# Optimization experiments

Hardware: AMD Instinct MI355X
Metric: run time of the kernel (lower is better)

The kernel has to match this reference:

```python
import jax, jax.numpy as jnp
import numpy as np

T = 512        # sentence length
V = 50000      # word vocab
NT = 50        # tag vocab
WD = 200       # word_dims
TD = 50        # tag_dims
U = 512        # lstm_units (per direction)
HID = 1024     # hidden_units
SOUT = 2       # struct_out
LOUT = 56      # label_out
NS = 8192      # number of struct span-sets
NL = 8192      # number of label span-sets
KS = 4         # struct_spans
KL = 3         # label_spans


def _spans(kl, kr, n, k):
    lefts = jax.random.randint(kl, (n, k), 1, T - 2)
    rights = jnp.minimum(lefts + jax.random.randint(kr, (n, k), 0, 16), T - 2)
    return lefts.astype(jnp.int32), rights.astype(jnp.int32)


def setup_inputs() -> dict:
    key = jax.random.key(0)
    ks = jax.random.split(key, 40)
    s = 0.02
    inp = {
        'word_inds': jax.random.randint(ks[0], (T,), 0, V).astype(jnp.int32),
        'tag_inds': jax.random.randint(ks[1], (T,), 0, NT).astype(jnp.int32),
        'struct_targets': jax.random.randint(ks[2], (NS,), 0, SOUT).astype(jnp.int32),
        'label_targets': jax.random.randint(ks[3], (NL,), 0, LOUT).astype(jnp.int32),
    }
    inp['struct_lefts'], inp['struct_rights'] = _spans(ks[4], ks[5], NS, KS)
    inp['label_lefts'], inp['label_rights'] = _spans(ks[6], ks[7], NL, KL)
    inp['W_word'] = jax.random.normal(ks[8], (V, WD), jnp.float32) * s
    inp['W_tag'] = jax.random.normal(ks[9], (NT, TD), jnp.float32) * s
    # LSTM params, PyTorch layout: W_ih [4U, in], W_hh [4U, U], bias [4U] (b_ih+b_hh fused)
    d0, d1 = WD + TD, 2 * U
    i = 10
    for name, din in [('l0f', d0), ('l0b', d0), ('l1f', d1), ('l1b', d1)]:
        inp['Wih_' + name] = jax.random.normal(ks[i], (4 * U, din), jnp.float32) * s; i += 1
        inp['Whh_' + name] = jax.random.normal(ks[i], (4 * U, U), jnp.float32) * s; i += 1
        inp['b_' + name] = jnp.zeros((4 * U,), jnp.float32)
    inp['Ws1'] = jax.random.normal(ks[i], (HID, 2 * KS * U), jnp.float32) * s; i += 1
    inp['bs1'] = jnp.zeros((HID,), jnp.float32)
    inp['Ws2'] = jax.random.normal(ks[i], (SOUT, HID), jnp.float32) * s; i += 1
    inp['bs2'] = jnp.zeros((SOUT,), jnp.float32)
    inp['Wl1'] = jax.random.normal(ks[i], (HID, 2 * KL * U), jnp.float32) * s; i += 1
    inp['bl1'] = jnp.zeros((HID,), jnp.float32)
    inp['Wl2'] = jax.random.normal(ks[i], (LOUT, HID), jnp.float32) * s; i += 1
    inp['bl2'] = jnp.zeros((LOUT,), jnp.float32)
    return inp


def _lstm_dir(x, Wih, Whh, b, reverse):
    # x: [T, Din] -> h sequence [T, U]; gate order i,f,g,o (PyTorch)
    xg = x @ Wih.T + b  # [T, 4U]
    u = Whh.shape[1]
    def step(carry, xt):
        h, c = carry
        g = xt + h @ Whh.T
        gi, gf, gg, go = jnp.split(g, 4)
        i = jax.nn.sigmoid(gi); f = jax.nn.sigmoid(gf)
        gg = jnp.tanh(gg); o = jax.nn.sigmoid(go)
        c = f * c + i * gg
        h = o * jnp.tanh(c)
        return (h, c), h
    init = (jnp.zeros((u,), x.dtype), jnp.zeros((u,), x.dtype))
    _, hs = jax.lax.scan(step, init, xg, reverse=reverse)
    return hs


def _span_loss(fwd, back, lefts, rights, targets, W1, b1, W2, b2):
    n = lefts.shape[0]
    f = fwd[rights] - fwd[lefts - 1]          # [N, K, U]
    bk = back[lefts] - back[rights + 1]       # [N, K, U]
    h = jnp.concatenate([f.reshape(n, -1), bk.reshape(n, -1)], axis=1)
    h = jax.nn.relu(h @ W1.T + b1)
    scores = h @ W2.T + b2
    logp = jax.nn.log_softmax(scores, axis=-1)
    return -jnp.take_along_axis(logp, targets[:, None], axis=1)[:, 0]


def reference(word_inds, tag_inds, struct_lefts, struct_rights, struct_targets,
              label_lefts, label_rights, label_targets,
              W_word, W_tag,
              Wih_l0f, Whh_l0f, b_l0f, Wih_l0b, Whh_l0b, b_l0b,
              Wih_l1f, Whh_l1f, b_l1f, Wih_l1b, Whh_l1b, b_l1b,
              Ws1, bs1, Ws2, bs2, Wl1, bl1, Wl2, bl2):
    x = jnp.concatenate([W_word[word_inds], W_tag[tag_inds]], axis=1)  # [T, WD+TD]
    h0 = jnp.concatenate([_lstm_dir(x, Wih_l0f, Whh_l0f, b_l0f, False),
                          _lstm_dir(x, Wih_l0b, Whh_l0b, b_l0b, True)], axis=1)
    out = jnp.concatenate([_lstm_dir(h0, Wih_l1f, Whh_l1f, b_l1f, False),
                           _lstm_dir(h0, Wih_l1b, Whh_l1b, b_l1b, True)], axis=1)  # [T, 2U]
    fwd, back = out[:, :U], out[:, U:]
    sl = _span_loss(fwd, back, struct_lefts, struct_rights, struct_targets, Ws1, bs1, Ws2, bs2)
    ll = _span_loss(fwd, back, label_lefts, label_rights, label_targets, Wl1, bl1, Wl2, bl2)
    return jnp.concatenate([sl, ll]).mean()
```

## Files before the change

### kernel.cpp

```cpp
#include <hip/hip_runtime.h>

using u16 = unsigned short;
using u32 = unsigned int;
typedef __attribute__((ext_vector_type(8))) short bf16x8;
typedef __attribute__((ext_vector_type(4))) float f32x4;

__device__ __forceinline__ u16 f2b(float f) {
  u32 u = __float_as_uint(f);
  return (u16)((u + 0x7fffu + ((u >> 16) & 1u)) >> 16);
}
__device__ __forceinline__ float b2fs(short v) { return __uint_as_float(((u32)(u16)v) << 16); }

static constexpr size_t HEX_SZ    = (size_t)513 * 512 * 4;
static constexpr size_t OFF_HEXF0 = 0;
static constexpr size_t OFF_HEXB0 = OFF_HEXF0 + HEX_SZ;
static constexpr size_t OFF_HEXF1 = OFF_HEXB0 + HEX_SZ;
static constexpr size_t OFF_HEXB1 = OFF_HEXF1 + HEX_SZ;
static constexpr size_t OFF_LACC  = OFF_HEXB1 + HEX_SZ;
static constexpr size_t ZERO_BYTES= OFF_LACC + 1024;
static constexpr size_t OFF_XB    = ZERO_BYTES;
static constexpr size_t OFF_WIH0F = OFF_XB    + (size_t)512*256*2;
static constexpr size_t OFF_WIH0B = OFF_WIH0F + (size_t)2048*256*2;
static constexpr size_t OFF_WIH1F = OFF_WIH0B + (size_t)2048*256*2;
static constexpr size_t OFF_WIH1B = OFF_WIH1F + (size_t)2048*1024*2;
static constexpr size_t OFF_BSALL = OFF_WIH1B + (size_t)2048*1024*2;
static constexpr size_t OFF_BLALL = OFF_BSALL + (size_t)8192*512*2;
static constexpr size_t OFF_HCAT0 = OFF_BLALL + (size_t)6144*512*2;
static constexpr size_t OFF_HCAT1 = OFF_HCAT0 + (size_t)512*1024*2;
static constexpr size_t OFF_XG0F  = OFF_HCAT1 + (size_t)512*1024*2;
static constexpr size_t OFF_XG0B  = OFF_XG0F  + (size_t)512*2048*4;
static constexpr size_t OFF_XG1F  = OFF_XG0B  + (size_t)512*2048*4;
static constexpr size_t OFF_XG1B  = OFF_XG1F  + (size_t)512*2048*4;
static constexpr size_t OFF_PFS   = OFF_XG1B  + (size_t)512*2048*4;
static constexpr size_t OFF_PBS   = OFF_PFS   + (size_t)512*4096*4;
static constexpr size_t OFF_PFL   = OFF_PBS   + (size_t)512*4096*4;
static constexpr size_t OFF_PBL   = OFF_PFL   + (size_t)512*3072*4;

__global__ __launch_bounds__(64) void k_embed(const int* __restrict__ wi, const int* __restrict__ ti,
                                              const float* __restrict__ Ww, const float* __restrict__ Wt,
                                              u16* __restrict__ x) {
  int t = blockIdx.x;
  int w = wi[t], tg = ti[t];
  for (int c = threadIdx.x; c < 256; c += 64) {
    float v = 0.f;
    if (c < 200) v = Ww[(size_t)w * 200 + c];
    else if (c < 250) v = Wt[(size_t)tg * 50 + (c - 200)];
    x[(size_t)t * 256 + c] = f2b(v);
  }
}

__global__ __launch_bounds__(256) void k_castpad(const float* __restrict__ src, u16* __restrict__ dst,
                                                 int K, int Kp, int total) {
  int i = blockIdx.x * 256 + threadIdx.x;
  if (i >= total) return;
  int n = i / Kp, k = i - n * Kp;
  dst[i] = (k < K) ? f2b(src[(size_t)n * K + k]) : (u16)0;
}

__global__ __launch_bounds__(256) void k_reorder(const float* __restrict__ src, u16* __restrict__ dst,
                                                 int NC, int total) {
  int i = blockIdx.x * 256 + threadIdx.x;
  if (i >= total) return;
  int u = i & 511;
  int nidx = i >> 9;
  int k = nidx >> 10, h = nidx & 1023;
  dst[i] = f2b(src[(size_t)h * NC + k * 512 + u]);
}

#define AST 40
__global__ __launch_bounds__(256) void k_gemm(const u16* __restrict__ A, int lda,
                                              const u16* __restrict__ B, int ldb,
                                              float* __restrict__ C, int ldc,
                                              const float* __restrict__ bias, int K) {
  __shared__ u16 As[128 * AST];
  __shared__ u16 Bs[128 * AST];
  int tid = threadIdx.x;
  int lane = tid & 63, wave = tid >> 6;
  int wm = wave >> 1, wn = wave & 1;
  int m0 = blockIdx.y * 128, n0 = blockIdx.x * 128;
  f32x4 z = {0.f, 0.f, 0.f, 0.f};
  f32x4 acc[4][4];
#pragma unroll
  for (int i = 0; i < 4; ++i)
#pragma unroll
    for (int j = 0; j < 4; ++j) acc[i][j] = z;

  for (int k0 = 0; k0 < K; k0 += 32) {
#pragma unroll
    for (int it = 0; it < 2; ++it) {
      int c = tid + it * 256;
      int row = c >> 2, cc = (c & 3) << 3;
      *(bf16x8*)&As[row * AST + cc] = *(const bf16x8*)&A[(size_t)(m0 + row) * lda + k0 + cc];
      *(bf16x8*)&Bs[row * AST + cc] = *(const bf16x8*)&B[(size_t)(n0 + row) * ldb + k0 + cc];
    }
    __syncthreads();
    int rA = lane & 15, kk = (lane >> 4) << 3;
    bf16x8 af[4], bg[4];
#pragma unroll
    for (int i = 0; i < 4; ++i) {
      af[i] = *(const bf16x8*)&As[(wm * 64 + i * 16 + rA) * AST + kk];
      bg[i] = *(const bf16x8*)&Bs[(wn * 64 + i * 16 + rA) * AST + kk];
    }
#pragma unroll
    for (int i = 0; i < 4; ++i)
#pragma unroll
      for (int j = 0; j < 4; ++j)
        acc[i][j] = __builtin_amdgcn_mfma_f32_16x16x32_bf16(af[i], bg[j], acc[i][j], 0, 0, 0);
    __syncthreads();
  }
  int rg = (lane >> 4) << 2;
#pragma unroll
  for (int i = 0; i < 4; ++i)
#pragma unroll
    for (int j = 0; j < 4; ++j) {
      int n = n0 + wn * 64 + j * 16 + (lane & 15);
      float bv = bias ? bias[n] : 0.f;
#pragma unroll
      for (int r = 0; r < 4; ++r) {
        int m = m0 + wm * 64 + i * 16 + rg + r;
        C[(size_t)m * ldc + n] = acc[i][j][r] + bv;
      }
    }
}

__global__ __launch_bounds__(256, 1) void k_lstm(const float* __restrict__ xg_f, const float* __restrict__ xg_b,
                                                 const float* __restrict__ whh_f, const float* __restrict__ whh_b,
                                                 u32* __restrict__ hex_f, u32* __restrict__ hex_b,
                                                 u16* __restrict__ hcat) {
  __shared__ __align__(16) u16 hshb[512];
  __shared__ float gl[128];
  int bid = blockIdx.x;
  int dir = bid >> 4, slice = bid & 15;
  const float* xg  = dir ? xg_b : xg_f;
  const float* whh = dir ? whh_b : whh_f;
  u32* hex = dir ? hex_b : hex_f;
  int u0 = slice * 32;
  int tid = threadIdx.x;
  int wave = tid >> 6, lane = tid & 63;
  int col = lane & 15, kgrp = lane >> 4;

  bf16x8 bfr[2][16];
#pragma unroll
  for (int ntl = 0; ntl < 2; ++ntl) {
    int n = (2 * wave + ntl) * 16 + col;
    int row = (n >> 5) * 512 + u0 + (n & 31);
    const float* wr = whh + (size_t)row * 512;
#pragma unroll
    for (int kt = 0; kt < 16; ++kt) {
      int k0 = kt * 32 + kgrp * 8;
      f32x4 w0 = *(const f32x4*)&wr[k0];
      f32x4 w1 = *(const f32x4*)&wr[k0 + 4];
      bf16x8 v;
      v[0] = (short)f2b(w0.x); v[1] = (short)f2b(w0.y);
      v[2] = (short)f2b(w0.z); v[3] = (short)f2b(w0.w);
      v[4] = (short)f2b(w1.x); v[5] = (short)f2b(w1.y);
      v[6] = (short)f2b(w1.z); v[7] = (short)f2b(w1.w);
      bfr[ntl][kt] = v;
    }
  }

  float creg = 0.f;
  for (int s = 0; s < 512; ++s) {
    int t = dir ? (511 - s) : s;
    int rrow = dir ? (t + 1) : t;

    float xga = 0.f, xgb2 = 0.f, xgc = 0.f, xgd = 0.f;
    if (tid < 32) {
      const float* xr = &xg[(size_t)t * 2048 + u0 + tid];
      xga = xr[0]; xgb2 = xr[512]; xgc = xr[1024]; xgd = xr[1536];
    }

    for (int i = tid; i < 512; i += 256) {
      u32 w;
      do {
        w = __hip_atomic_load(&hex[(size_t)rrow * 512 + i], __ATOMIC_RELAXED, __HIP_MEMORY_SCOPE_AGENT);
      } while ((w & 0xFFFFu) != (u32)s);
      hshb[i] = (u16)(w >> 16);
    }
    __syncthreads();

    f32x4 z4 = {0.f, 0.f, 0.f, 0.f};
    f32x4 acc0[4], acc1[4];
#pragma unroll
    for (int q = 0; q < 4; ++q) { acc0[q] = z4; acc1[q] = z4; }
#pragma unroll
    for (int kt = 0; kt < 16; ++kt) {
      bf16x8 a = *(const bf16x8*)&hshb[kt * 32 + kgrp * 8];
      acc0[kt & 3] = __builtin_amdgcn_mfma_f32_16x16x32_bf16(a, bfr[0][kt], acc0[kt & 3], 0, 0, 0);
      acc1[kt & 3] = __builtin_amdgcn_mfma_f32_16x16x32_bf16(a, bfr[1][kt], acc1[kt & 3], 0, 0, 0);
    }
    if (lane < 16) {
      float v0 = acc0[0].x + acc0[1].x + acc0[2].x + acc0[3].x;
      float v1 = acc1[0].x + acc1[1].x + acc1[2].x + acc1[3].x;
      gl[(2 * wave) * 16 + lane] = v0;
      gl[(2 * wave + 1) * 16 + lane] = v1;
    }
    __syncthreads();

    if (tid < 32) {
      float gi = gl[tid] + xga, gf = gl[32 + tid] + xgb2, gg = gl[64 + tid] + xgc, go = gl[96 + tid] + xgd;
      float iv = 1.f / (1.f + __expf(-gi));
      float fv = 1.f / (1.f + __expf(-gf));
      float gv = tanhf(gg);
      float ov = 1.f / (1.f + __expf(-go));
      creg = fv * creg + iv * gv;
      float h = ov * tanhf(creg);
      u16 hb16 = f2b(h);
      int wrow = dir ? t : (t + 1);
      u32 word = ((u32)hb16 << 16) | (u32)(s + 1);
      __hip_atomic_store(&hex[(size_t)wrow * 512 + u0 + tid], word, __ATOMIC_RELAXED, __HIP_MEMORY_SCOPE_AGENT);
      hcat[(size_t)t * 1024 + dir * 512 + u0 + tid] = hb16;
    }
  }
}

template <int KSP, int C>
__global__ __launch_bounds__(256) void k_span_loss(const float* __restrict__ Pf, const float* __restrict__ Pb,
                                                   const int* __restrict__ lefts, const int* __restrict__ rights,
                                                   const int* __restrict__ tgts, const float* __restrict__ b1,
                                                   const float* __restrict__ W2, const float* __restrict__ b2,
                                                   float* __restrict__ loss_acc) {
  constexpr int NP = KSP * 1024;
  __shared__ float hid[4][1024];
  __shared__ float sc[4][64];
  int tid = threadIdx.x;
  int n0 = blockIdx.x * 4;
  int d = tid * 4;
  f32x4 bv = *(const f32x4*)&b1[d];
#pragma unroll
  for (int ss = 0; ss < 4; ++ss) {
    int n = n0 + ss;
    f32x4 acc = bv;
#pragma unroll
    for (int k = 0; k < KSP; ++k) {
      int l = lefts[n * KSP + k], r = rights[n * KSP + k];
      f32x4 a1 = *(const f32x4*)&Pf[(size_t)r * NP + k * 1024 + d];
      f32x4 a2 = *(const f32x4*)&Pf[(size_t)(l - 1) * NP + k * 1024 + d];
      f32x4 a3 = *(const f32x4*)&Pb[(size_t)l * NP + k * 1024 + d];
      f32x4 a4 = *(const f32x4*)&Pb[(size_t)(r + 1) * NP + k * 1024 + d];
      acc += a1 - a2 + a3 - a4;
    }
    acc.x = fmaxf(acc.x, 0.f); acc.y = fmaxf(acc.y, 0.f);
    acc.z = fmaxf(acc.z, 0.f); acc.w = fmaxf(acc.w, 0.f);
    *(f32x4*)&hid[ss][d] = acc;
  }
  __syncthreads();
  int wave = tid >> 6, lane = tid & 63;
  for (int c = wave; c < C; c += 4) {
    float p0 = 0.f, p1 = 0.f, p2 = 0.f, p3 = 0.f;
    for (int i = lane; i < 1024; i += 64) {
      float w = W2[(size_t)c * 1024 + i];
      p0 += hid[0][i] * w; p1 += hid[1][i] * w; p2 += hid[2][i] * w; p3 += hid[3][i] * w;
    }
#pragma unroll
    for (int o = 32; o; o >>= 1) {
      p0 += __shfl_xor(p0, o); p1 += __shfl_xor(p1, o);
      p2 += __shfl_xor(p2, o); p3 += __shfl_xor(p3, o);
    }
    if (lane == 0) {
      sc[0][c] = p0 + b2[c]; sc[1][c] = p1 + b2[c];
      sc[2][c] = p2 + b2[c]; sc[3][c] = p3 + b2[c];
    }
  }
  __syncthreads();
  {
    int s = wave;
    float v = (lane < C) ? sc[s][lane] : -1e30f;
    float m = v;
#pragma unroll
    for (int o = 32; o; o >>= 1) m = fmaxf(m, __shfl_xor(m, o));
    float e = (lane < C) ? __expf(v - m) : 0.f;
#pragma unroll
    for (int o = 32; o; o >>= 1) e += __shfl_xor(e, o);
    if (lane == 0) {
      int tg = tgts[n0 + s];
      float loss = m + __logf(e) - sc[s][tg];
      atomicAdd(&loss_acc[(n0 + s) & 255], loss);
    }
  }
}

__global__ __launch_bounds__(256) void k_finalize(const float* __restrict__ acc, float* __restrict__ out) {
  int tid = threadIdx.x;
  __shared__ float s[4];
  float v = acc[tid];
#pragma unroll
  for (int o = 32; o; o >>= 1) v += __shfl_xor(v, o);
  if ((tid & 63) == 0) s[tid >> 6] = v;
  __syncthreads();
  if (tid == 0) out[0] = (s[0] + s[1] + s[2] + s[3]) * (1.0f / 16384.0f);
}

extern "C" void kernel_launch(void* const* d_in, const int* in_sizes, int n_in,
                              void* d_out, int out_size, void* d_ws, size_t ws_size,
                              hipStream_t stream) {
  (void)in_sizes; (void)n_in; (void)out_size; (void)ws_size;
  const int* word_inds = (const int*)d_in[0];
  const int* tag_inds  = (const int*)d_in[1];
  const int* s_tgt = (const int*)d_in[2];
  const int* l_tgt = (const int*)d_in[3];
  const int* s_l = (const int*)d_in[4];
  const int* s_r = (const int*)d_in[5];
  const int* l_l = (const int*)d_in[6];
  const int* l_r = (const int*)d_in[7];
  const float* W_word  = (const float*)d_in[8];
  const float* W_tag   = (const float*)d_in[9];
  const float* Wih_l0f = (const float*)d_in[10];
  const float* Whh_l0f = (const float*)d_in[11];
  const float* b_l0f   = (const float*)d_in[12];
  const float* Wih_l0b = (const float*)d_in[13];
  const float* Whh_l0b = (const float*)d_in[14];
  const float* b_l0b   = (const float*)d_in[15];
  const float* Wih_l1f = (const float*)d_in[16];
  const float* Whh_l1f = (const float*)d_in[17];
  const float* b_l1f   = (const float*)d_in[18];
  const float* Wih_l1b = (const float*)d_in[19];
  const float* Whh_l1b = (const float*)d_in[20];
  const float* b_l1b   = (const float*)d_in[21];
  const float* Ws1 = (const float*)d_in[22];
  const float* bs1 = (const float*)d_in[23];
  const float* Ws2 = (const float*)d_in[24];
  const float* bs2 = (const float*)d_in[25];
  const float* Wl1 = (const float*)d_in[26];
  const float* bl1 = (const float*)d_in[27];
  const float* Wl2 = (const float*)d_in[28];
  const float* bl2 = (const float*)d_in[29];

  char* ws = (char*)d_ws;
  u32* hexf0 = (u32*)(ws + OFF_HEXF0);
  u32* hexb0 = (u32*)(ws + OFF_HEXB0);
  u32* hexf1 = (u32*)(ws + OFF_HEXF1);
  u32* hexb1 = (u32*)(ws + OFF_HEXB1);
  float* lacc = (float*)(ws + OFF_LACC);
  u16* xb    = (u16*)(ws + OFF_XB);
  u16* wih0f = (u16*)(ws + OFF_WIH0F);
  u16* wih0b = (u16*)(ws + OFF_WIH0B);
  u16* wih1f = (u16*)(ws + OFF_WIH1F);
  u16* wih1b = (u16*)(ws + OFF_WIH1B);
  u16* bsall = (u16*)(ws + OFF_BSALL);
  u16* blall = (u16*)(ws + OFF_BLALL);
  u16* hcat0 = (u16*)(ws + OFF_HCAT0);
  u16* hcat1 = (u16*)(ws + OFF_HCAT1);
  float* xg0f = (float*)(ws + OFF_XG0F);
  float* xg0b = (float*)(ws + OFF_XG0B);
  float* xg1f = (float*)(ws + OFF_XG1F);
  float* xg1b = (float*)(ws + OFF_XG1B);
  float* Pfs = (float*)(ws + OFF_PFS);
  float* Pbs = (float*)(ws + OFF_PBS);
  float* Pfl = (float*)(ws + OFF_PFL);
  float* Pbl = (float*)(ws + OFF_PBL);

  hipMemsetAsync(ws, 0, ZERO_BYTES, stream);

  k_embed<<<512, 64, 0, stream>>>(word_inds, tag_inds, W_word, W_tag, xb);
  k_castpad<<<(2048 * 256) / 256, 256, 0, stream>>>(Wih_l0f, wih0f, 250, 256, 2048 * 256);
  k_castpad<<<(2048 * 256) / 256, 256, 0, stream>>>(Wih_l0b, wih0b, 250, 256, 2048 * 256);
  k_castpad<<<(2048 * 1024) / 256, 256, 0, stream>>>(Wih_l1f, wih1f, 1024, 1024, 2048 * 1024);
  k_castpad<<<(2048 * 1024) / 256, 256, 0, stream>>>(Wih_l1b, wih1b, 1024, 1024, 2048 * 1024);
  k_reorder<<<(8 * 1024 * 512) / 256, 256, 0, stream>>>(Ws1, bsall, 4096, 8 * 1024 * 512);
  k_reorder<<<(6 * 1024 * 512) / 256, 256, 0, stream>>>(Wl1, blall, 3072, 6 * 1024 * 512);

  k_gemm<<<dim3(16, 4), 256, 0, stream>>>(xb, 256, wih0f, 256, xg0f, 2048, b_l0f, 256);
  k_gemm<<<dim3(16, 4), 256, 0, stream>>>(xb, 256, wih0b, 256, xg0b, 2048, b_l0b, 256);
  k_lstm<<<32, 256, 0, stream>>>(xg0f, xg0b, Whh_l0f, Whh_l0b, hexf0, hexb0, hcat0);
  k_gemm<<<dim3(16, 4), 256, 0, stream>>>(hcat0, 1024, wih1f, 1024, xg1f, 2048, b_l1f, 1024);
  k_gemm<<<dim3(16, 4), 256, 0, stream>>>(hcat0, 1024, wih1b, 1024, xg1b, 2048, b_l1b, 1024);
  k_lstm<<<32, 256, 0, stream>>>(xg1f, xg1b, Whh_l1f, Whh_l1b, hexf1, hexb1, hcat1);

  k_gemm<<<dim3(32, 4), 256, 0, stream>>>(hcat1, 1024, bsall, 512, Pfs, 4096, nullptr, 512);
  k_gemm<<<dim3(32, 4), 256, 0, stream>>>(hcat1 + 512, 1024, bsall + (size_t)4096 * 512, 512, Pbs, 4096, nullptr, 512);
  k_gemm<<<dim3(24, 4), 256, 0, stream>>>(hcat1, 1024, blall, 512, Pfl, 3072, nullptr, 512);
  k_gemm<<<dim3(24, 4), 256, 0, stream>>>(hcat1 + 512, 1024, blall + (size_t)3072 * 512, 512, Pbl, 3072, nullptr, 512);

  k_span_loss<4, 2><<<2048, 256, 0, stream>>>(Pfs, Pbs, s_l, s_r, s_tgt, bs1, Ws2, bs2, lacc);
  k_span_loss<3, 56><<<2048, 256, 0, stream>>>(Pfl, Pbl, l_l, l_r, l_tgt, bl1, Wl2, bl2, lacc);
  k_finalize<<<1, 256, 0, stream>>>(lacc, (float*)d_out);
}
```

Before: 2.459 ms.

## Restructure LSTM step to per-wave sync-free and fuse launches with overlapped weight prep

Each wave of the LSTM kernel now polls the full hidden vector itself with 64-bit tagged loads into its own double-buffered LDS slot. The four gates for its 8 units are combined with shuffles and fast rcp/exp activations, which removes both __syncthreads per timestep. The layer-1 and span-projection weight cast/reorder work runs in extra blocks of the layer-0 LSTM launch, so it overlaps the latency-bound recurrence. The paired GEMMs, the projection GEMMs and the span-loss kernels are merged into single launches. Each wave redundantly fetches the hidden state, which adds polling traffic, and the fast tanh approximation may change numerics slightly.

```diff
diff --git a/kernel.cpp b/kernel.cpp
--- a/kernel.cpp
+++ b/kernel.cpp
@@ -2,6 +2,7 @@
 
 using u16 = unsigned short;
 using u32 = unsigned int;
+using u64 = unsigned long long;
 typedef __attribute__((ext_vector_type(8))) short bf16x8;
 typedef __attribute__((ext_vector_type(4))) float f32x4;
 
@@ -9,7 +10,6 @@
   u32 u = __float_as_uint(f);
   return (u16)((u + 0x7fffu + ((u >> 16) & 1u)) >> 16);
 }
-__device__ __forceinline__ float b2fs(short v) { return __uint_as_float(((u32)(u16)v) << 16); }
 
 static constexpr size_t HEX_SZ    = (size_t)513 * 512 * 4;
 static constexpr size_t OFF_HEXF0 = 0;
@@ -49,35 +49,27 @@
   }
 }
 
-__global__ __launch_bounds__(256) void k_castpad(const float* __restrict__ src, u16* __restrict__ dst,
-                                                 int K, int Kp, int total) {
-  int i = blockIdx.x * 256 + threadIdx.x;
-  if (i >= total) return;
-  int n = i / Kp, k = i - n * Kp;
-  dst[i] = (k < K) ? f2b(src[(size_t)n * K + k]) : (u16)0;
-}
-
-__global__ __launch_bounds__(256) void k_reorder(const float* __restrict__ src, u16* __restrict__ dst,
-                                                 int NC, int total) {
-  int i = blockIdx.x * 256 + threadIdx.x;
-  if (i >= total) return;
-  int u = i & 511;
-  int nidx = i >> 9;
-  int k = nidx >> 10, h = nidx & 1023;
-  dst[i] = f2b(src[(size_t)h * NC + k * 512 + u]);
+__global__ __launch_bounds__(256) void k_prep0(const float* __restrict__ sf, const float* __restrict__ sb,
+                                               u16* __restrict__ df, u16* __restrict__ db) {
+  int stride = gridDim.x * 256;
+  for (int i = blockIdx.x * 256 + threadIdx.x; i < 2048 * 256; i += stride) {
+    int n = i >> 8, k = i & 255;
+    df[i] = (k < 250) ? f2b(sf[(size_t)n * 250 + k]) : (u16)0;
+    db[i] = (k < 250) ? f2b(sb[(size_t)n * 250 + k]) : (u16)0;
+  }
 }
 
 #define AST 40
-__global__ __launch_bounds__(256) void k_gemm(const u16* __restrict__ A, int lda,
-                                              const u16* __restrict__ B, int ldb,
-                                              float* __restrict__ C, int ldc,
-                                              const float* __restrict__ bias, int K) {
+__device__ __forceinline__ void gemm_body(const u16* __restrict__ A, int lda,
+                                          const u16* __restrict__ B, int ldb,
+                                          float* __restrict__ C, int ldc,
+                                          const float* __restrict__ bias, int K,
+                                          int m0, int n0) {
   __shared__ u16 As[128 * AST];
   __shared__ u16 Bs[128 * AST];
   int tid = threadIdx.x;
   int lane = tid & 63, wave = tid >> 6;
   int wm = wave >> 1, wn = wave & 1;
-  int m0 = blockIdx.y * 128, n0 = blockIdx.x * 128;
   f32x4 z = {0.f, 0.f, 0.f, 0.f};
   f32x4 acc[4][4];
 #pragma unroll
@@ -123,12 +115,33 @@
     }
 }
 
-__global__ __launch_bounds__(256, 1) void k_lstm(const float* __restrict__ xg_f, const float* __restrict__ xg_b,
-                                                 const float* __restrict__ whh_f, const float* __restrict__ whh_b,
-                                                 u32* __restrict__ hex_f, u32* __restrict__ hex_b,
-                                                 u16* __restrict__ hcat) {
-  __shared__ __align__(16) u16 hshb[512];
-  __shared__ float gl[128];
+__global__ __launch_bounds__(256) void k_gemm2(const u16* A, int lda,
+                                               const u16* B0, const u16* B1, int ldb,
+                                               float* C0, float* C1, int ldc,
+                                               const float* bias0, const float* bias1, int K) {
+  int z = blockIdx.z;
+  gemm_body(A, lda, z ? B1 : B0, ldb, z ? C1 : C0, ldc, z ? bias1 : bias0, K,
+            blockIdx.y * 128, blockIdx.x * 128);
+}
+
+__global__ __launch_bounds__(256) void k_proj(const u16* hcat1, const u16* bsall, const u16* blall,
+                                              float* Pfs, float* Pbs, float* Pfl, float* Pbl) {
+  int z = blockIdx.z;
+  if (z >= 2 && blockIdx.x >= 24) return;
+  const u16* A = (z & 1) ? (hcat1 + 512) : hcat1;
+  const u16* B; float* C; int N;
+  if (z == 0)      { B = bsall;                        C = Pfs; N = 4096; }
+  else if (z == 1) { B = bsall + (size_t)4096 * 512;   C = Pbs; N = 4096; }
+  else if (z == 2) { B = blall;                        C = Pfl; N = 3072; }
+  else             { B = blall + (size_t)3072 * 512;   C = Pbl; N = 3072; }
+  gemm_body(A, 1024, B, 512, C, N, nullptr, 512, blockIdx.y * 128, blockIdx.x * 128);
+}
+
+__device__ __forceinline__ void lstm_body(const float* __restrict__ xg_f, const float* __restrict__ xg_b,
+                                          const float* __restrict__ whh_f, const float* __restrict__ whh_b,
+                                          u32* __restrict__ hex_f, u32* __restrict__ hex_b,
+                                          u16* __restrict__ hcat) {
+  __shared__ __align__(16) u16 hw[4][2][512];
   int bid = blockIdx.x;
   int dir = bid >> 4, slice = bid & 15;
   const float* xg  = dir ? xg_b : xg_f;
@@ -138,12 +151,13 @@
   int tid = threadIdx.x;
   int wave = tid >> 6, lane = tid & 63;
   int col = lane & 15, kgrp = lane >> 4;
+  int uw = u0 + 8 * wave;
 
   bf16x8 bfr[2][16];
 #pragma unroll
   for (int ntl = 0; ntl < 2; ++ntl) {
-    int n = (2 * wave + ntl) * 16 + col;
-    int row = (n >> 5) * 512 + u0 + (n & 31);
+    int gate = 2 * ntl + (col >> 3);
+    int row = gate * 512 + uw + (col & 7);
     const float* wr = whh + (size_t)row * 512;
 #pragma unroll
     for (int kt = 0; kt < 16; ++kt) {
@@ -159,72 +173,114 @@
     }
   }
 
+  const u64 TAGM = 0x0000FFFF0000FFFFull;
   float creg = 0.f;
   for (int s = 0; s < 512; ++s) {
     int t = dir ? (511 - s) : s;
     int rrow = dir ? (t + 1) : t;
-
-    float xga = 0.f, xgb2 = 0.f, xgc = 0.f, xgd = 0.f;
-    if (tid < 32) {
-      const float* xr = &xg[(size_t)t * 2048 + u0 + tid];
-      xga = xr[0]; xgb2 = xr[512]; xgc = xr[1024]; xgd = xr[1536];
-    }
-
-    for (int i = tid; i < 512; i += 256) {
-      u32 w;
-      do {
-        w = __hip_atomic_load(&hex[(size_t)rrow * 512 + i], __ATOMIC_RELAXED, __HIP_MEMORY_SCOPE_AGENT);
-      } while ((w & 0xFFFFu) != (u32)s);
-      hshb[i] = (u16)(w >> 16);
-    }
-    __syncthreads();
-
+    int par = s & 1;
+
+    const float* xr = &xg[(size_t)t * 2048 + uw + (lane & 7)];
+    float xga = xr[0], xgb2 = xr[512], xgc = xr[1024], xgd = xr[1536];
+
+    const u64* hp = (const u64*)(hex + (size_t)rrow * 512) + lane * 4;
+    u64 expct = (u64)(u32)s | ((u64)(u32)s << 32);
+    u64 w0, w1, w2, w3;
+    do {
+      w0 = __hip_atomic_load(hp + 0, __ATOMIC_RELAXED, __HIP_MEMORY_SCOPE_AGENT);
+      w1 = __hip_atomic_load(hp + 1, __ATOMIC_RELAXED, __HIP_MEMORY_SCOPE_AGENT);
+      w2 = __hip_atomic_load(hp + 2, __ATOMIC_RELAXED, __HIP_MEMORY_SCOPE_AGENT);
+      w3 = __hip_atomic_load(hp + 3, __ATOMIC_RELAXED, __HIP_MEMORY_SCOPE_AGENT);
+    } while (((w0 & TAGM) != expct) | ((w1 & TAGM) != expct) |
+             ((w2 & TAGM) != expct) | ((w3 & TAGM) != expct));
+
+    bf16x8 hv;
+    hv[0] = (short)(u16)(w0 >> 16); hv[1] = (short)(u16)(w0 >> 48);
+    hv[2] = (short)(u16)(w1 >> 16); hv[3] = (short)(u16)(w1 >> 48);
+    hv[4] = (short)(u16)(w2 >> 16); hv[5] = (short)(u16)(w2 >> 48);
+    hv[6] = (short)(u16)(w3 >> 16); hv[7] = (short)(u16)(w3 >> 48);
+    *(bf16x8*)&hw[wave][par][lane * 8] = hv;
+
+    const u16* hb = &hw[wave][par][0];
     f32x4 z4 = {0.f, 0.f, 0.f, 0.f};
     f32x4 acc0[4], acc1[4];
 #pragma unroll
     for (int q = 0; q < 4; ++q) { acc0[q] = z4; acc1[q] = z4; }
 #pragma unroll
     for (int kt = 0; kt < 16; ++kt) {
-      bf16x8 a = *(const bf16x8*)&hshb[kt * 32 + kgrp * 8];
+      bf16x8 a = *(const bf16x8*)&hb[kt * 32 + kgrp * 8];
       acc0[kt & 3] = __builtin_amdgcn_mfma_f32_16x16x32_bf16(a, bfr[0][kt], acc0[kt & 3], 0, 0, 0);
       acc1[kt & 3] = __builtin_amdgcn_mfma_f32_16x16x32_bf16(a, bfr[1][kt], acc1[kt & 3], 0, 0, 0);
     }
-    if (lane < 16) {
-      float v0 = acc0[0].x + acc0[1].x + acc0[2].x + acc0[3].x;
-      float v1 = acc1[0].x + acc1[1].x + acc1[2].x + acc1[3].x;
-      gl[(2 * wave) * 16 + lane] = v0;
-      gl[(2 * wave + 1) * 16 + lane] = v1;
-    }
-    __syncthreads();
-
-    if (tid < 32) {
-      float gi = gl[tid] + xga, gf = gl[32 + tid] + xgb2, gg = gl[64 + tid] + xgc, go = gl[96 + tid] + xgd;
-      float iv = 1.f / (1.f + __expf(-gi));
-      float fv = 1.f / (1.f + __expf(-gf));
-      float gv = tanhf(gg);
-      float ov = 1.f / (1.f + __expf(-go));
+    float v0 = acc0[0].x + acc0[1].x + acc0[2].x + acc0[3].x;
+    float v1 = acc1[0].x + acc1[1].x + acc1[2].x + acc1[3].x;
+    float gfv = __shfl_xor(v0, 8);
+    float gov = __shfl_xor(v1, 8);
+    if (lane < 8) {
+      float gi = v0 + xga, gf = gfv + xgb2, gg = v1 + xgc, go = gov + xgd;
+      float iv = __builtin_amdgcn_rcpf(1.f + __expf(-gi));
+      float fv = __builtin_amdgcn_rcpf(1.f + __expf(-gf));
+      float gv = 1.f - 2.f * __builtin_amdgcn_rcpf(__expf(2.f * gg) + 1.f);
+      float ov = __builtin_amdgcn_rcpf(1.f + __expf(-go));
       creg = fv * creg + iv * gv;
-      float h = ov * tanhf(creg);
+      float h = ov * (1.f - 2.f * __builtin_amdgcn_rcpf(__expf(2.f * creg) + 1.f));
       u16 hb16 = f2b(h);
       int wrow = dir ? t : (t + 1);
       u32 word = ((u32)hb16 << 16) | (u32)(s + 1);
-      __hip_atomic_store(&hex[(size_t)wrow * 512 + u0 + tid], word, __ATOMIC_RELAXED, __HIP_MEMORY_SCOPE_AGENT);
-      hcat[(size_t)t * 1024 + dir * 512 + u0 + tid] = hb16;
-    }
+      __hip_atomic_store(&hex[(size_t)wrow * 512 + uw + lane], word, __ATOMIC_RELAXED, __HIP_MEMORY_SCOPE_AGENT);
+      hcat[(size_t)t * 1024 + dir * 512 + uw + lane] = hb16;
+    }
+  }
+}
+
+__global__ __launch_bounds__(256, 1) void k_lstm(const float* __restrict__ xg_f, const float* __restrict__ xg_b,
+                                                 const float* __restrict__ whh_f, const float* __restrict__ whh_b,
+                                                 u32* __restrict__ hex_f, u32* __restrict__ hex_b,
+                                                 u16* __restrict__ hcat) {
+  lstm_body(xg_f, xg_b, whh_f, whh_b, hex_f, hex_b, hcat);
+}
+
+__global__ __launch_bounds__(256, 1) void k_lstm_fused(const float* __restrict__ xg_f, const float* __restrict__ xg_b,
+                                                       const float* __restrict__ whh_f, const float* __restrict__ whh_b,
+                                                       u32* __restrict__ hex_f, u32* __restrict__ hex_b,
+                                                       u16* __restrict__ hcat,
+                                                       const float* __restrict__ Wih_l1f, const float* __restrict__ Wih_l1b,
+                                                       u16* __restrict__ wih1f, u16* __restrict__ wih1b,
+                                                       const float* __restrict__ Ws1, u16* __restrict__ bsall,
+                                                       const float* __restrict__ Wl1, u16* __restrict__ blall) {
+  if (blockIdx.x < 32) {
+    lstm_body(xg_f, xg_b, whh_f, whh_b, hex_f, hex_b, hcat);
+    return;
+  }
+  int pid = blockIdx.x - 32;
+  int nb = gridDim.x - 32;
+  int i0 = pid * 256 + threadIdx.x, stride = nb * 256;
+  for (int i = i0; i < 2048 * 1024; i += stride) {
+    wih1f[i] = f2b(Wih_l1f[i]);
+    wih1b[i] = f2b(Wih_l1b[i]);
+  }
+  for (int i = i0; i < 8 * 1024 * 512; i += stride) {
+    int u = i & 511, nidx = i >> 9, k = nidx >> 10, h = nidx & 1023;
+    bsall[i] = f2b(Ws1[(size_t)h * 4096 + k * 512 + u]);
+  }
+  for (int i = i0; i < 6 * 1024 * 512; i += stride) {
+    int u = i & 511, nidx = i >> 9, k = nidx >> 10, h = nidx & 1023;
+    blall[i] = f2b(Wl1[(size_t)h * 3072 + k * 512 + u]);
   }
 }
 
 template <int KSP, int C>
-__global__ __launch_bounds__(256) void k_span_loss(const float* __restrict__ Pf, const float* __restrict__ Pb,
-                                                   const int* __restrict__ lefts, const int* __restrict__ rights,
-                                                   const int* __restrict__ tgts, const float* __restrict__ b1,
-                                                   const float* __restrict__ W2, const float* __restrict__ b2,
-                                                   float* __restrict__ loss_acc) {
+__device__ __forceinline__ void span_body(int blk,
+                                          const float* __restrict__ Pf, const float* __restrict__ Pb,
+                                          const int* __restrict__ lefts, const int* __restrict__ rights,
+                                          const int* __restrict__ tgts, const float* __restrict__ b1,
+                                          const float* __restrict__ W2, const float* __restrict__ b2,
+                                          float* __restrict__ loss_acc) {
   constexpr int NP = KSP * 1024;
   __shared__ float hid[4][1024];
   __shared__ float sc[4][64];
   int tid = threadIdx.x;
-  int n0 = blockIdx.x * 4;
+  int n0 = blk * 4;
   int d = tid * 4;
   f32x4 bv = *(const f32x4*)&b1[d];
 #pragma unroll
@@ -278,6 +334,19 @@
       atomicAdd(&loss_acc[(n0 + s) & 255], loss);
     }
   }
+}
+
+__global__ __launch_bounds__(256) void k_span_fused(const float* Pfs, const float* Pbs,
+                                                    const int* s_l, const int* s_r, const int* s_tgt,
+                                                    const float* bs1, const float* Ws2, const float* bs2,
+                                                    const float* Pfl, const float* Pbl,
+                                                    const int* l_l, const int* l_r, const int* l_tgt,
+                                                    const float* bl1, const float* Wl2, const float* bl2,
+                                                    float* lacc) {
+  if (blockIdx.x < 2048)
+    span_body<4, 2>(blockIdx.x, Pfs, Pbs, s_l, s_r, s_tgt, bs1, Ws2, bs2, lacc);
+  else
+    span_body<3, 56>(blockIdx.x - 2048, Pfl, Pbl, l_l, l_r, l_tgt, bl1, Wl2, bl2, lacc);
 }
 
 __global__ __launch_bounds__(256) void k_finalize(const float* __restrict__ acc, float* __restrict__ out) {
@@ -353,26 +422,17 @@
   hipMemsetAsync(ws, 0, ZERO_BYTES, stream);
 
   k_embed<<<512, 64, 0, stream>>>(word_inds, tag_inds, W_word, W_tag, xb);
-  k_castpad<<<(2048 * 256) / 256, 256, 0, stream>>>(Wih_l0f, wih0f, 250, 256, 2048 * 256);
-  k_castpad<<<(2048 * 256) / 256, 256, 0, stream>>>(Wih_l0b, wih0b, 250, 256, 2048 * 256);
-  k_castpad<<<(2048 * 1024) / 256, 256, 0, stream>>>(Wih_l1f, wih1f, 1024, 1024, 2048 * 1024);
-  k_castpad<<<(2048 * 1024) / 256, 256, 0, stream>>>(Wih_l1b, wih1b, 1024, 1024, 2048 * 1024);
-  k_reorder<<<(8 * 1024 * 512) / 256, 256, 0, stream>>>(Ws1, bsall, 4096, 8 * 1024 * 512);
-  k_reorder<<<(6 * 1024 * 512) / 256, 256, 0, stream>>>(Wl1, blall, 3072, 6 * 1024 * 512);
-
-  k_gemm<<<dim3(16, 4), 256, 0, stream>>>(xb, 256, wih0f, 256, xg0f, 2048, b_l0f, 256);
-  k_gemm<<<dim3(16, 4), 256, 0, stream>>>(xb, 256, wih0b, 256, xg0b, 2048, b_l0b, 256);
-  k_lstm<<<32, 256, 0, stream>>>(xg0f, xg0b, Whh_l0f, Whh_l0b, hexf0, hexb0, hcat0);
-  k_gemm<<<dim3(16, 4), 256, 0, stream>>>(hcat0, 1024, wih1f, 1024, xg1f, 2048, b_l1f, 1024);
-  k_gemm<<<dim3(16, 4), 256, 0, stream>>>(hcat0, 1024, wih1b, 1024, xg1b, 2048, b_l1b, 1024);
+  k_prep0<<<512, 256, 0, stream>>>(Wih_l0f, Wih_l0b, wih0f, wih0b);
+
+  k_gemm2<<<dim3(16, 4, 2), 256, 0, stream>>>(xb, 256, wih0f, wih0b, 256, xg0f, xg0b, 2048, b_l0f, b_l0b, 256);
+  k_lstm_fused<<<544, 256, 0, stream>>>(xg0f, xg0b, Whh_l0f, Whh_l0b, hexf0, hexb0, hcat0,
+                                        Wih_l1f, Wih_l1b, wih1f, wih1b, Ws1, bsall, Wl1, blall);
+  k_gemm2<<<dim3(16, 4, 2), 256, 0, stream>>>(hcat0, 1024, wih1f, wih1b, 1024, xg1f, xg1b, 2048, b_l1f, b_l1b, 1024);
   k_lstm<<<32, 256, 0, stream>>>(xg1f, xg1b, Whh_l1f, Whh_l1b, hexf1, hexb1, hcat1);
 
-  k_gemm<<<dim3(32, 4), 256, 0, stream>>>(hcat1, 1024, bsall, 512, Pfs, 4096, nullptr, 512);
-  k_gemm<<<dim3(32, 4), 256, 0, stream>>>(hcat1 + 512, 1024, bsall + (size_t)4096 * 512, 512, Pbs, 4096, nullptr, 512);
-  k_gemm<<<dim3(24, 4), 256, 0, stream>>>(hcat1, 1024, blall, 512, Pfl, 3072, nullptr, 512);
-  k_gemm<<<dim3(24, 4), 256, 0, stream>>>(hcat1 + 512, 1024, blall + (size_t)3072 * 512, 512, Pbl, 3072, nullptr, 512);
-
-  k_span_loss<4, 2><<<2048, 256, 0, stream>>>(Pfs, Pbs, s_l, s_r, s_tgt, bs1, Ws2, bs2, lacc);
-  k_span_loss<3, 56><<<2048, 256, 0, stream>>>(Pfl, Pbl, l_l, l_r, l_tgt, bl1, Wl2, bl2, lacc);
+  k_proj<<<dim3(32, 4, 4), 256, 0, stream>>>(hcat1, bsall, blall, Pfs, Pbs, Pfl, Pbl);
+
+  k_span_fused<<<4096, 256, 0, stream>>>(Pfs, Pbs, s_l, s_r, s_tgt, bs1, Ws2, bs2,
+                                         Pfl, Pbl, l_l, l_r, l_tgt, bl1, Wl2, bl2, lacc);
   k_finalize<<<1, 256, 0, stream>>>(lacc, (float*)d_out);
 }
```

After: 2.686 ms. 9.2% more time.
